# Performance work log

Hardware: AMD Instinct MI355X
Metric: run time of the kernel (lower is better)

Reference implementation:

```python
import jax, jax.numpy as jnp
import numpy as np

N = 100000      # nodes
E = 1_600_000   # edges (avg degree 16)
DIMS = [(64, 64), (64, 64), (64, 40)]  # gnn_layers [64,64,64,40]


def setup_inputs() -> dict:
    key = jax.random.key(0)
    ks = jax.random.split(key, 2 + 3 * len(DIMS))
    inp = {
        "x": jax.random.normal(ks[0], (N, DIMS[0][0]), jnp.float32),
        "edge_index": jax.random.randint(ks[1], (2, E), 0, N),
    }
    k = 2
    for i, (din, dout) in enumerate(DIMS):
        s = 1.0 / np.sqrt(din)
        inp[f"Wl{i}"] = jax.random.uniform(ks[k], (din, dout), jnp.float32, -s, s); k += 1
        inp[f"bl{i}"] = jax.random.uniform(ks[k], (dout,), jnp.float32, -s, s); k += 1
        inp[f"Wr{i}"] = jax.random.uniform(ks[k], (din, dout), jnp.float32, -s, s); k += 1
    return inp


def _sage_conv(x, src, dst, Wl, bl, Wr):
    # PyG SAGEConv (mean aggr): out = lin_l(mean_{j in N(i)} x_j) + lin_r(x_i)
    deg = jax.ops.segment_sum(jnp.ones((src.shape[0],), x.dtype), dst, num_segments=N)
    agg = jax.ops.segment_sum(x[src], dst, num_segments=N)  # [N, din] scatter-add
    agg = agg / jnp.clip(deg, 1.0)[:, None]                  # mean; isolated nodes -> 0
    return agg @ Wl + bl + x @ Wr


def reference(x, edge_index, Wl0, bl0, Wr0, Wl1, bl1, Wr1, Wl2, bl2, Wr2):
    src, dst = edge_index[0], edge_index[1]
    h = x
    params = [(Wl0, bl0, Wr0), (Wl1, bl1, Wr1), (Wl2, bl2, Wr2)]
    for i, (Wl, bl, Wr) in enumerate(params):
        h = _sage_conv(h, src, dst, Wl, bl, Wr)
        if i != len(params) - 1:
            h = jax.nn.relu(h)
            # F.dropout with training=False is identity (eval mode)
    return jax.nn.log_softmax(h, axis=1)
```

## Files before the change

### kernel.cpp

```cpp
#include <hip/hip_runtime.h>
#include <math.h>

#define ACT_RELU 0
#define ACT_LSM  1
#define BSH 8
#define MAXNB 512
#define MPAD 80

typedef __attribute__((ext_vector_type(8))) short bf16x8;
typedef __attribute__((ext_vector_type(4))) float f32x4;

__device__ __forceinline__ unsigned f2bf(float f) {
  unsigned u = __float_as_uint(f);
  u += 0x7fffu + ((u >> 16) & 1u);
  return u >> 16;
}
__device__ __forceinline__ float bflo(unsigned u) { return __uint_as_float(u << 16); }
__device__ __forceinline__ float bfhi(unsigned u) { return __uint_as_float(u & 0xffff0000u); }

__global__ void k_zero(int* __restrict__ p, int n) {
  int i = blockIdx.x * 256 + threadIdx.x;
  if (i < n) p[i] = 0;
}

__global__ void k_histB(const int* __restrict__ dst, int* __restrict__ bucket_cnt,
                        int E, int NB) {
  __shared__ int cntL[MAXNB];
  int t = threadIdx.x;
  for (int b = t; b < NB; b += 256) cntL[b] = 0;
  __syncthreads();
  int e0 = blockIdx.x * 4096;
  int e1 = min(e0 + 4096, E);
  for (int i = e0 + t; i < e1; i += 256) atomicAdd(&cntL[dst[i] >> BSH], 1);
  __syncthreads();
  for (int b = t; b < NB; b += 256)
    if (cntL[b]) atomicAdd(&bucket_cnt[b], cntL[b]);
}

__global__ void k_bscan(const int* __restrict__ bucket_cnt, int* __restrict__ bucket_base,
                        int* __restrict__ bucket_cursor, int NB) {
  __shared__ int sm[MAXNB];
  int t = threadIdx.x;
  sm[t] = (t < NB) ? bucket_cnt[t] : 0;
  __syncthreads();
  for (int off = 1; off < MAXNB; off <<= 1) {
    int x = (t >= off) ? sm[t - off] : 0;
    __syncthreads();
    sm[t] += x;
    __syncthreads();
  }
  int ex = (t == 0) ? 0 : sm[t - 1];
  if (t <= NB) bucket_base[t] = ex;
  if (t < NB) bucket_cursor[t] = ex;
}

__global__ void k_partition(const int* __restrict__ src, const int* __restrict__ dst,
                            int* __restrict__ bucket_cursor, unsigned* __restrict__ tmp,
                            int E, int NB) {
  __shared__ int cntL[MAXNB];
  __shared__ int baseL[MAXNB];
  int t = threadIdx.x;
  for (int b = t; b < NB; b += 256) cntL[b] = 0;
  __syncthreads();
  int e0 = blockIdx.x * 4096;
  int e1 = min(e0 + 4096, E);
  for (int i = e0 + t; i < e1; i += 256) atomicAdd(&cntL[dst[i] >> BSH], 1);
  __syncthreads();
  for (int b = t; b < NB; b += 256) {
    int c = cntL[b];
    baseL[b] = c ? atomicAdd(&bucket_cursor[b], c) : 0;
    cntL[b] = 0;
  }
  __syncthreads();
  for (int i = e0 + t; i < e1; i += 256) {
    int s = src[i], d = dst[i];
    int b = d >> BSH;
    int r = atomicAdd(&cntL[b], 1);
    tmp[baseL[b] + r] = ((unsigned)s << 8) | (unsigned)(d & 255);
  }
}

__global__ void __launch_bounds__(256) k_bmake(const unsigned* __restrict__ tmp,
                                               const int* __restrict__ bucket_base,
                                               int* __restrict__ row_ptr,
                                               int* __restrict__ edge_src,
                                               int N, int E, int NB) {
  __shared__ int cntL[256];
  __shared__ int scanL[256];
  int b = blockIdx.x;
  int t = threadIdx.x;
  int e0 = bucket_base[b], e1 = bucket_base[b + 1];
  cntL[t] = 0;
  __syncthreads();
  for (int i = e0 + t; i < e1; i += 256) atomicAdd(&cntL[tmp[i] & 255], 1);
  __syncthreads();
  int v = cntL[t];
  scanL[t] = v;
  __syncthreads();
  for (int off = 1; off < 256; off <<= 1) {
    int x = (t >= off) ? scanL[t - off] : 0;
    __syncthreads();
    scanL[t] += x;
    __syncthreads();
  }
  int exc = scanL[t] - v;
  int node = (b << BSH) + t;
  if (node < N) row_ptr[node] = e0 + exc;
  if (b == NB - 1 && t == 0) row_ptr[N] = E;
  __syncthreads();
  cntL[t] = e0 + exc;
  __syncthreads();
  for (int i = e0 + t; i < e1; i += 256) {
    unsigned e = tmp[i];
    int p = atomicAdd(&cntL[e & 255], 1);
    edge_src[p] = (int)(e >> 8);
  }
}

__global__ void k_hist(const int* __restrict__ dst, int* __restrict__ cnt, int E) {
  int i = blockIdx.x * blockDim.x + threadIdx.x;
  if (i < E) atomicAdd(&cnt[dst[i]], 1);
}

__global__ void k_scan_part(const int* __restrict__ cnt, int* __restrict__ bsum, int M) {
  __shared__ int sm[256];
  int t = threadIdx.x;
  int base = blockIdx.x * 2048 + t * 8;
  int s = 0;
#pragma unroll
  for (int j = 0; j < 8; ++j) { int i = base + j; if (i < M) s += cnt[i]; }
  sm[t] = s;
  __syncthreads();
  for (int off = 128; off > 0; off >>= 1) {
    if (t < off) sm[t] += sm[t + off];
    __syncthreads();
  }
  if (t == 0) bsum[blockIdx.x] = sm[0];
}

__global__ void k_scan_mid(const int* __restrict__ bsum, int* __restrict__ boff, int nb) {
  int l = threadIdx.x;
  int v = (l < nb) ? bsum[l] : 0;
  int inc = v;
  for (int off = 1; off < 64; off <<= 1) {
    int u = __shfl_up(inc, off);
    if (l >= off) inc += u;
  }
  if (l < nb) boff[l] = inc - v;
}

__global__ void k_scan_final(const int* __restrict__ cnt, const int* __restrict__ boff,
                             int* __restrict__ row_ptr, int* __restrict__ cursor, int M) {
  __shared__ int sm[256];
  int t = threadIdx.x;
  int base = blockIdx.x * 2048 + t * 8;
  int v[8];
  int s = 0;
#pragma unroll
  for (int j = 0; j < 8; ++j) { int i = base + j; v[j] = (i < M) ? cnt[i] : 0; s += v[j]; }
  sm[t] = s;
  __syncthreads();
  for (int off = 1; off < 256; off <<= 1) {
    int x = (t >= off) ? sm[t - off] : 0;
    __syncthreads();
    sm[t] += x;
    __syncthreads();
  }
  int run = boff[blockIdx.x] + sm[t] - s;
#pragma unroll
  for (int j = 0; j < 8; ++j) {
    int i = base + j;
    if (i < M) { row_ptr[i] = run; cursor[i] = run; }
    run += v[j];
  }
}

__global__ void k_fill(const int* __restrict__ src, const int* __restrict__ dst,
                       int* __restrict__ cursor, int* __restrict__ edge_src, int E) {
  int i = blockIdx.x * blockDim.x + threadIdx.x;
  if (i < E) {
    int d = dst[i];
    int p = atomicAdd(&cursor[d], 1);
    edge_src[p] = src[i];
  }
}

__global__ void __launch_bounds__(256) k_cast(const float* __restrict__ x,
                                              unsigned short* __restrict__ xb, int n) {
  int i = blockIdx.x * 256 + threadIdx.x;
  if (i * 8 < n) {
    const float4* p = (const float4*)(x + (size_t)i * 8);
    float4 a = p[0], b = p[1];
    uint4 w;
    w.x = f2bf(a.x) | (f2bf(a.y) << 16);
    w.y = f2bf(a.z) | (f2bf(a.w) << 16);
    w.z = f2bf(b.x) | (f2bf(b.y) << 16);
    w.w = f2bf(b.z) | (f2bf(b.w) << 16);
    *(uint4*)(xb + (size_t)i * 8) = w;
  }
}

__device__ __forceinline__ void prepw_one(const float* Wl, const float* Wr,
                                          unsigned short* Wb, int fi, int DOUT, int NT) {
  int k7 = fi & 7;
  int kb = (fi >> 3) & 3;
  int c16 = (fi >> 5) & 15;
  int rest = fi >> 9;
  int nt = rest % NT;
  int kb5 = rest / NT;
  int k = kb5 * 32 + kb * 8 + k7;
  int nn = nt * 16 + c16;
  float v = 0.f;
  if (nn < DOUT) v = (k < 64) ? Wl[k * DOUT + nn] : Wr[(k - 64) * DOUT + nn];
  Wb[fi] = (unsigned short)f2bf(v);
}

__global__ void k_prepw3(const float* __restrict__ Wl0, const float* __restrict__ Wr0,
                         unsigned short* __restrict__ Wb0,
                         const float* __restrict__ Wl1, const float* __restrict__ Wr1,
                         unsigned short* __restrict__ Wb1,
                         const float* __restrict__ Wl2, const float* __restrict__ Wr2,
                         unsigned short* __restrict__ Wb2) {
  int i = blockIdx.x * 256 + threadIdx.x;
  if (i < 8192) prepw_one(Wl0, Wr0, Wb0, i, 64, 4);
  else if (i < 16384) prepw_one(Wl1, Wr1, Wb1, i - 8192, 64, 4);
  else if (i < 22528) prepw_one(Wl2, Wr2, Wb2, i - 16384, 40, 3);
}

template <int DOUT, int ACT>
__global__ void __launch_bounds__(256) k_layer(const unsigned short* __restrict__ h,
                                               const int* __restrict__ row_ptr,
                                               const int* __restrict__ edge_src,
                                               const unsigned short* __restrict__ Wb,
                                               const float* __restrict__ bias,
                                               void* __restrict__ outv, int n) {
  constexpr int NT = (DOUT + 15) / 16;
  __shared__ unsigned short meanL[4][8 * MPAD];
  int t = threadIdx.x;
  int w = t >> 6, lane = t & 63;
  int r0 = (blockIdx.x * 4 + w) * 8;
  int g = lane & 7;
  int node = lane >> 3;

  {
    int i = r0 + node;
    float a[8];
#pragma unroll
    for (int c = 0; c < 8; ++c) a[c] = 0.f;
    float scale = 0.f;
    if (i < n) {
      int rp0 = row_ptr[i], rp1 = row_ptr[i + 1];
      int deg = rp1 - rp0;
      scale = (deg > 0) ? (1.0f / (float)deg) : 0.f;
      for (int base = 0; base < deg; base += 8) {
        int idx = rp0 + base + g;
        int sv = (idx < rp1) ? edge_src[idx] : 0;
        int cnt = min(8, deg - base);
        uint4 v0, v1, v2, v3, v4, v5, v6, v7;
#pragma unroll
        for (int e = 0; e < 8; ++e) {
          int s = __shfl(sv, (lane & ~7) | e);
          const uint4* p = (const uint4*)(h + (size_t)s * 64) + g;
          if (e == 0 && e < cnt) v0 = *p;
          if (e == 1 && e < cnt) v1 = *p;
          if (e == 2 && e < cnt) v2 = *p;
          if (e == 3 && e < cnt) v3 = *p;
          if (e == 4 && e < cnt) v4 = *p;
          if (e == 5 && e < cnt) v5 = *p;
          if (e == 6 && e < cnt) v6 = *p;
          if (e == 7 && e < cnt) v7 = *p;
        }
#define ACCUM(vv, ee)                                                   \
        if ((ee) < cnt) {                                               \
          a[0] += bflo(vv.x); a[1] += bfhi(vv.x);                       \
          a[2] += bflo(vv.y); a[3] += bfhi(vv.y);                       \
          a[4] += bflo(vv.z); a[5] += bfhi(vv.z);                       \
          a[6] += bflo(vv.w); a[7] += bfhi(vv.w);                       \
        }
        ACCUM(v0, 0) ACCUM(v1, 1) ACCUM(v2, 2) ACCUM(v3, 3)
        ACCUM(v4, 4) ACCUM(v5, 5) ACCUM(v6, 6) ACCUM(v7, 7)
#undef ACCUM
      }
    }
    uint4 wv;
    wv.x = f2bf(a[0] * scale) | (f2bf(a[1] * scale) << 16);
    wv.y = f2bf(a[2] * scale) | (f2bf(a[3] * scale) << 16);
    wv.z = f2bf(a[4] * scale) | (f2bf(a[5] * scale) << 16);
    wv.w = f2bf(a[6] * scale) | (f2bf(a[7] * scale) << 16);
    *(uint4*)&meanL[w][node * MPAD + g * 8] = wv;
  }
  __threadfence_block();

  int c = lane & 15;
  int c8 = c & 7;
  int kb = lane >> 4;
  bf16x8 af[4];
  af[0] = *(const bf16x8*)&meanL[w][c8 * MPAD + kb * 8];
  af[1] = *(const bf16x8*)&meanL[w][c8 * MPAD + 32 + kb * 8];
  int row = r0 + c8;
  if (row >= n) row = n - 1;
  size_t rb = (size_t)row * 64 + kb * 8;
  af[2] = *(const bf16x8*)(h + rb);
  af[3] = *(const bf16x8*)(h + rb + 32);

  f32x4 acc[NT];
#pragma unroll
  for (int nt = 0; nt < NT; ++nt) acc[nt] = (f32x4){0.f, 0.f, 0.f, 0.f};
#pragma unroll
  for (int s = 0; s < 4; ++s) {
    bf16x8 bft[NT];
#pragma unroll
    for (int nt = 0; nt < NT; ++nt)
      bft[nt] = *(const bf16x8*)&Wb[(((s * NT + nt) * 16 + c) * 4 + kb) * 8];
#pragma unroll
    for (int nt = 0; nt < NT; ++nt)
      acc[nt] = __builtin_amdgcn_mfma_f32_16x16x32_bf16(af[s], bft[nt], acc[nt], 0, 0, 0);
  }

  int rbase = r0 + kb * 4;
  bool rowv = (kb < 2);
  if (ACT == ACT_RELU) {
    unsigned short* out = (unsigned short*)outv;
#pragma unroll
    for (int nt = 0; nt < NT; ++nt) {
      float bval = bias[nt * 16 + c];
#pragma unroll
      for (int r = 0; r < 4; ++r) {
        int R = rbase + r;
        if (rowv && R < n) {
          float v = fmaxf(acc[nt][r] + bval, 0.f);
          out[(size_t)R * DOUT + nt * 16 + c] = (unsigned short)f2bf(v);
        }
      }
    }
  } else {
    float* out = (float*)outv;
    float bv[NT];
#pragma unroll
    for (int nt = 0; nt < NT; ++nt) bv[nt] = ((nt * 16 + c) < DOUT) ? bias[nt * 16 + c] : 0.f;
#pragma unroll
    for (int r = 0; r < 4; ++r) {
      int R = rbase + r;
      float v[NT];
      float m = -INFINITY;
#pragma unroll
      for (int nt = 0; nt < NT; ++nt) {
        bool valid = (nt * 16 + c) < DOUT;
        v[nt] = valid ? (acc[nt][r] + bv[nt]) : -INFINITY;
        m = fmaxf(m, v[nt]);
      }
#pragma unroll
      for (int off = 1; off < 16; off <<= 1) m = fmaxf(m, __shfl_xor(m, off));
      float es = 0.f;
#pragma unroll
      for (int nt = 0; nt < NT; ++nt)
        if ((nt * 16 + c) < DOUT) es += expf(v[nt] - m);
#pragma unroll
      for (int off = 1; off < 16; off <<= 1) es += __shfl_xor(es, off);
      float lse = logf(es);
      if (rowv && R < n) {
#pragma unroll
        for (int nt = 0; nt < NT; ++nt)
          if ((nt * 16 + c) < DOUT) out[(size_t)R * DOUT + nt * 16 + c] = v[nt] - m - lse;
      }
    }
  }
}

extern "C" void kernel_launch(void* const* d_in, const int* in_sizes, int n_in,
                              void* d_out, int out_size, void* d_ws, size_t ws_size,
                              hipStream_t stream) {
  const float* x   = (const float*)d_in[0];
  const int*   ei  = (const int*)d_in[1];
  const float* Wl0 = (const float*)d_in[2];
  const float* bl0 = (const float*)d_in[3];
  const float* Wr0 = (const float*)d_in[4];
  const float* Wl1 = (const float*)d_in[5];
  const float* bl1 = (const float*)d_in[6];
  const float* Wr1 = (const float*)d_in[7];
  const float* Wl2 = (const float*)d_in[8];
  const float* bl2 = (const float*)d_in[9];
  const float* Wr2 = (const float*)d_in[10];
  float* out = (float*)d_out;

  int N = in_sizes[0] / 64;
  int E = in_sizes[1] / 2;
  int M = N + 1;
  int NB = (N + 255) >> BSH;
  const int* src = ei;
  const int* dst = ei + E;

  char* p = (char*)d_ws;
  auto alloc = [&](size_t bytes) {
    char* r = p;
    p += (bytes + 255) & ~(size_t)255;
    return r;
  };
  int* cnt      = (int*)alloc((size_t)M * 4);
  int* row_ptr  = (int*)alloc((size_t)M * 4);
  int* cursor   = (int*)alloc((size_t)M * 4);
  int* bsum     = (int*)alloc(256 * 4);
  int* boff     = (int*)alloc(256 * 4);
  int* bk_cnt   = (int*)alloc((MAXNB + 1) * 4);
  int* bk_base  = (int*)alloc((MAXNB + 1) * 4);
  int* bk_cur   = (int*)alloc((MAXNB + 1) * 4);
  int* edge_src = (int*)alloc((size_t)E * 4);
  size_t szR1 = (size_t)E * 4 > (size_t)N * 128 ? (size_t)E * 4 : (size_t)N * 128;
  char* R1              = alloc(szR1);
  unsigned short* hbA   = (unsigned short*)alloc((size_t)N * 128);
  unsigned short* Wb0   = (unsigned short*)alloc(128 * 64 * 2);
  unsigned short* Wb1   = (unsigned short*)alloc(128 * 64 * 2);
  unsigned short* Wb2   = (unsigned short*)alloc(128 * 48 * 2);
  if ((size_t)(p - (char*)d_ws) > ws_size) return;

  bool bucketed = (NB <= MAXNB) && (N < (1 << 24));
  int eb4 = (E + 4095) / 4096;

  k_prepw3<<<(22528 + 255) / 256, 256, 0, stream>>>(Wl0, Wr0, Wb0, Wl1, Wr1, Wb1,
                                                    Wl2, Wr2, Wb2);

  if (bucketed) {
    k_zero<<<(MAXNB + 256) / 256, 256, 0, stream>>>(bk_cnt, MAXNB + 1);
    k_histB<<<eb4, 256, 0, stream>>>(dst, bk_cnt, E, NB);
    k_bscan<<<1, MAXNB, 0, stream>>>(bk_cnt, bk_base, bk_cur, NB);
    k_partition<<<eb4, 256, 0, stream>>>(src, dst, bk_cur, (unsigned*)R1, E, NB);
    k_bmake<<<NB, 256, 0, stream>>>((const unsigned*)R1, bk_base, row_ptr, edge_src, N, E, NB);
  } else {
    k_zero<<<(M + 255) / 256, 256, 0, stream>>>(cnt, M);
    k_hist<<<(E + 255) / 256, 256, 0, stream>>>(dst, cnt, E);
    int nb = (M + 2047) / 2048;
    k_scan_part<<<nb, 256, 0, stream>>>(cnt, bsum, M);
    k_scan_mid<<<1, 64, 0, stream>>>(bsum, boff, nb);
    k_scan_final<<<nb, 256, 0, stream>>>(cnt, boff, row_ptr, cursor, M);
    k_fill<<<(E + 255) / 256, 256, 0, stream>>>(src, dst, cursor, edge_src, E);
  }

  unsigned short* xb  = (unsigned short*)R1;
  unsigned short* hbB = (unsigned short*)R1;

  int cb = (N * 64 / 8 + 255) / 256;
  int gb = (N + 31) / 32;

  k_cast<<<cb, 256, 0, stream>>>(x, xb, N * 64);
  k_layer<64, ACT_RELU><<<gb, 256, 0, stream>>>(xb, row_ptr, edge_src, Wb0, bl0, hbA, N);
  k_layer<64, ACT_RELU><<<gb, 256, 0, stream>>>(hbA, row_ptr, edge_src, Wb1, bl1, hbB, N);
  k_layer<40, ACT_LSM><<<gb, 256, 0, stream>>>(hbB, row_ptr, edge_src, Wb2, bl2, out, N);
}
```

Measured before the change: 211.8 us.

## Fuse preprocessing kernels, deterministic per-block partition offsets, 16 rows per wave

The bucket-count zeroing moves into the weight-prep kernel, and the x-to-bf16 cast moves into the histogram kernel. Per-block bucket counts are now stored and prefix-scanned by a new kernel, so the partition pass no longer recounts edges or does global atomics. The temporary edge buffer gets its own allocation instead of aliasing the cast buffer, and each wave in the layer kernel now handles 16 rows, so all 16 MFMA rows are used instead of 8. The cost is an extra scan launch, more workspace for the per-block tables, and twice the gather work per wave, which may hurt latency hiding.

```diff
diff --git a/kernel.cpp b/kernel.cpp
--- a/kernel.cpp
+++ b/kernel.cpp
@@ -17,188 +17,6 @@
 }
 __device__ __forceinline__ float bflo(unsigned u) { return __uint_as_float(u << 16); }
 __device__ __forceinline__ float bfhi(unsigned u) { return __uint_as_float(u & 0xffff0000u); }
-
-__global__ void k_zero(int* __restrict__ p, int n) {
-  int i = blockIdx.x * 256 + threadIdx.x;
-  if (i < n) p[i] = 0;
-}
-
-__global__ void k_histB(const int* __restrict__ dst, int* __restrict__ bucket_cnt,
-                        int E, int NB) {
-  __shared__ int cntL[MAXNB];
-  int t = threadIdx.x;
-  for (int b = t; b < NB; b += 256) cntL[b] = 0;
-  __syncthreads();
-  int e0 = blockIdx.x * 4096;
-  int e1 = min(e0 + 4096, E);
-  for (int i = e0 + t; i < e1; i += 256) atomicAdd(&cntL[dst[i] >> BSH], 1);
-  __syncthreads();
-  for (int b = t; b < NB; b += 256)
-    if (cntL[b]) atomicAdd(&bucket_cnt[b], cntL[b]);
-}
-
-__global__ void k_bscan(const int* __restrict__ bucket_cnt, int* __restrict__ bucket_base,
-                        int* __restrict__ bucket_cursor, int NB) {
-  __shared__ int sm[MAXNB];
-  int t = threadIdx.x;
-  sm[t] = (t < NB) ? bucket_cnt[t] : 0;
-  __syncthreads();
-  for (int off = 1; off < MAXNB; off <<= 1) {
-    int x = (t >= off) ? sm[t - off] : 0;
-    __syncthreads();
-    sm[t] += x;
-    __syncthreads();
-  }
-  int ex = (t == 0) ? 0 : sm[t - 1];
-  if (t <= NB) bucket_base[t] = ex;
-  if (t < NB) bucket_cursor[t] = ex;
-}
-
-__global__ void k_partition(const int* __restrict__ src, const int* __restrict__ dst,
-                            int* __restrict__ bucket_cursor, unsigned* __restrict__ tmp,
-                            int E, int NB) {
-  __shared__ int cntL[MAXNB];
-  __shared__ int baseL[MAXNB];
-  int t = threadIdx.x;
-  for (int b = t; b < NB; b += 256) cntL[b] = 0;
-  __syncthreads();
-  int e0 = blockIdx.x * 4096;
-  int e1 = min(e0 + 4096, E);
-  for (int i = e0 + t; i < e1; i += 256) atomicAdd(&cntL[dst[i] >> BSH], 1);
-  __syncthreads();
-  for (int b = t; b < NB; b += 256) {
-    int c = cntL[b];
-    baseL[b] = c ? atomicAdd(&bucket_cursor[b], c) : 0;
-    cntL[b] = 0;
-  }
-  __syncthreads();
-  for (int i = e0 + t; i < e1; i += 256) {
-    int s = src[i], d = dst[i];
-    int b = d >> BSH;
-    int r = atomicAdd(&cntL[b], 1);
-    tmp[baseL[b] + r] = ((unsigned)s << 8) | (unsigned)(d & 255);
-  }
-}
-
-__global__ void __launch_bounds__(256) k_bmake(const unsigned* __restrict__ tmp,
-                                               const int* __restrict__ bucket_base,
-                                               int* __restrict__ row_ptr,
-                                               int* __restrict__ edge_src,
-                                               int N, int E, int NB) {
-  __shared__ int cntL[256];
-  __shared__ int scanL[256];
-  int b = blockIdx.x;
-  int t = threadIdx.x;
-  int e0 = bucket_base[b], e1 = bucket_base[b + 1];
-  cntL[t] = 0;
-  __syncthreads();
-  for (int i = e0 + t; i < e1; i += 256) atomicAdd(&cntL[tmp[i] & 255], 1);
-  __syncthreads();
-  int v = cntL[t];
-  scanL[t] = v;
-  __syncthreads();
-  for (int off = 1; off < 256; off <<= 1) {
-    int x = (t >= off) ? scanL[t - off] : 0;
-    __syncthreads();
-    scanL[t] += x;
-    __syncthreads();
-  }
-  int exc = scanL[t] - v;
-  int node = (b << BSH) + t;
-  if (node < N) row_ptr[node] = e0 + exc;
-  if (b == NB - 1 && t == 0) row_ptr[N] = E;
-  __syncthreads();
-  cntL[t] = e0 + exc;
-  __syncthreads();
-  for (int i = e0 + t; i < e1; i += 256) {
-    unsigned e = tmp[i];
-    int p = atomicAdd(&cntL[e & 255], 1);
-    edge_src[p] = (int)(e >> 8);
-  }
-}
-
-__global__ void k_hist(const int* __restrict__ dst, int* __restrict__ cnt, int E) {
-  int i = blockIdx.x * blockDim.x + threadIdx.x;
-  if (i < E) atomicAdd(&cnt[dst[i]], 1);
-}
-
-__global__ void k_scan_part(const int* __restrict__ cnt, int* __restrict__ bsum, int M) {
-  __shared__ int sm[256];
-  int t = threadIdx.x;
-  int base = blockIdx.x * 2048 + t * 8;
-  int s = 0;
-#pragma unroll
-  for (int j = 0; j < 8; ++j) { int i = base + j; if (i < M) s += cnt[i]; }
-  sm[t] = s;
-  __syncthreads();
-  for (int off = 128; off > 0; off >>= 1) {
-    if (t < off) sm[t] += sm[t + off];
-    __syncthreads();
-  }
-  if (t == 0) bsum[blockIdx.x] = sm[0];
-}
-
-__global__ void k_scan_mid(const int* __restrict__ bsum, int* __restrict__ boff, int nb) {
-  int l = threadIdx.x;
-  int v = (l < nb) ? bsum[l] : 0;
-  int inc = v;
-  for (int off = 1; off < 64; off <<= 1) {
-    int u = __shfl_up(inc, off);
-    if (l >= off) inc += u;
-  }
-  if (l < nb) boff[l] = inc - v;
-}
-
-__global__ void k_scan_final(const int* __restrict__ cnt, const int* __restrict__ boff,
-                             int* __restrict__ row_ptr, int* __restrict__ cursor, int M) {
-  __shared__ int sm[256];
-  int t = threadIdx.x;
-  int base = blockIdx.x * 2048 + t * 8;
-  int v[8];
-  int s = 0;
-#pragma unroll
-  for (int j = 0; j < 8; ++j) { int i = base + j; v[j] = (i < M) ? cnt[i] : 0; s += v[j]; }
-  sm[t] = s;
-  __syncthreads();
-  for (int off = 1; off < 256; off <<= 1) {
-    int x = (t >= off) ? sm[t - off] : 0;
-    __syncthreads();
-    sm[t] += x;
-    __syncthreads();
-  }
-  int run = boff[blockIdx.x] + sm[t] - s;
-#pragma unroll
-  for (int j = 0; j < 8; ++j) {
-    int i = base + j;
-    if (i < M) { row_ptr[i] = run; cursor[i] = run; }
-    run += v[j];
-  }
-}
-
-__global__ void k_fill(const int* __restrict__ src, const int* __restrict__ dst,
-                       int* __restrict__ cursor, int* __restrict__ edge_src, int E) {
-  int i = blockIdx.x * blockDim.x + threadIdx.x;
-  if (i < E) {
-    int d = dst[i];
-    int p = atomicAdd(&cursor[d], 1);
-    edge_src[p] = src[i];
-  }
-}
-
-__global__ void __launch_bounds__(256) k_cast(const float* __restrict__ x,
-                                              unsigned short* __restrict__ xb, int n) {
-  int i = blockIdx.x * 256 + threadIdx.x;
-  if (i * 8 < n) {
-    const float4* p = (const float4*)(x + (size_t)i * 8);
-    float4 a = p[0], b = p[1];
-    uint4 w;
-    w.x = f2bf(a.x) | (f2bf(a.y) << 16);
-    w.y = f2bf(a.z) | (f2bf(a.w) << 16);
-    w.z = f2bf(b.x) | (f2bf(b.y) << 16);
-    w.w = f2bf(b.z) | (f2bf(b.w) << 16);
-    *(uint4*)(xb + (size_t)i * 8) = w;
-  }
-}
 
 __device__ __forceinline__ void prepw_one(const float* Wl, const float* Wr,
                                           unsigned short* Wb, int fi, int DOUT, int NT) {
@@ -220,11 +38,219 @@
                          const float* __restrict__ Wl1, const float* __restrict__ Wr1,
                          unsigned short* __restrict__ Wb1,
                          const float* __restrict__ Wl2, const float* __restrict__ Wr2,
-                         unsigned short* __restrict__ Wb2) {
+                         unsigned short* __restrict__ Wb2,
+                         int* __restrict__ bk_cnt) {
   int i = blockIdx.x * 256 + threadIdx.x;
   if (i < 8192) prepw_one(Wl0, Wr0, Wb0, i, 64, 4);
   else if (i < 16384) prepw_one(Wl1, Wr1, Wb1, i - 8192, 64, 4);
   else if (i < 22528) prepw_one(Wl2, Wr2, Wb2, i - 16384, 40, 3);
+  if (i <= MAXNB) bk_cnt[i] = 0;
+}
+
+__global__ void __launch_bounds__(256) k_histB(const int* __restrict__ dst,
+                                               const float* __restrict__ x,
+                                               unsigned short* __restrict__ xb,
+                                               int* __restrict__ bucket_cnt,
+                                               int* __restrict__ bk_blk,
+                                               int E, int NB, int NBLK, int nx8) {
+  __shared__ int cntL[MAXNB];
+  int t = threadIdx.x;
+  for (int i = blockIdx.x * 256 + t; i < nx8; i += gridDim.x * 256) {
+    const float4* p = (const float4*)(x + (size_t)i * 8);
+    float4 a = p[0], b = p[1];
+    uint4 w;
+    w.x = f2bf(a.x) | (f2bf(a.y) << 16);
+    w.y = f2bf(a.z) | (f2bf(a.w) << 16);
+    w.z = f2bf(b.x) | (f2bf(b.y) << 16);
+    w.w = f2bf(b.z) | (f2bf(b.w) << 16);
+    *(uint4*)(xb + (size_t)i * 8) = w;
+  }
+  for (int b = t; b < NB; b += 256) cntL[b] = 0;
+  __syncthreads();
+  int e0 = blockIdx.x * 4096;
+  int e1 = min(e0 + 4096, E);
+  for (int i = e0 + t; i < e1; i += 256) atomicAdd(&cntL[dst[i] >> BSH], 1);
+  __syncthreads();
+  for (int b = t; b < NB; b += 256) {
+    int c = cntL[b];
+    bk_blk[b * NBLK + blockIdx.x] = c;
+    if (c) atomicAdd(&bucket_cnt[b], c);
+  }
+}
+
+__global__ void k_bscan(const int* __restrict__ bucket_cnt, int* __restrict__ bucket_base,
+                        int NB) {
+  __shared__ int sm[MAXNB];
+  int t = threadIdx.x;
+  sm[t] = (t < NB) ? bucket_cnt[t] : 0;
+  __syncthreads();
+  for (int off = 1; off < MAXNB; off <<= 1) {
+    int x = (t >= off) ? sm[t - off] : 0;
+    __syncthreads();
+    sm[t] += x;
+    __syncthreads();
+  }
+  int ex = (t == 0) ? 0 : sm[t - 1];
+  if (t <= NB) bucket_base[t] = ex;
+}
+
+__global__ void k_bscan2(const int* __restrict__ bk_blk, const int* __restrict__ bucket_base,
+                         int* __restrict__ base_blk, int NBLK) {
+  __shared__ int sm[512];
+  int b = blockIdx.x;
+  int t = threadIdx.x;
+  int v = (t < NBLK) ? bk_blk[b * NBLK + t] : 0;
+  sm[t] = v;
+  __syncthreads();
+  for (int off = 1; off < 512; off <<= 1) {
+    int x = (t >= off) ? sm[t - off] : 0;
+    __syncthreads();
+    sm[t] += x;
+    __syncthreads();
+  }
+  if (t < NBLK) base_blk[b * NBLK + t] = bucket_base[b] + sm[t] - v;
+}
+
+__global__ void k_partition(const int* __restrict__ src, const int* __restrict__ dst,
+                            const int* __restrict__ base_blk, unsigned* __restrict__ tmp,
+                            int E, int NB, int NBLK) {
+  __shared__ int curL[MAXNB];
+  int t = threadIdx.x;
+  for (int b = t; b < NB; b += 256) curL[b] = base_blk[b * NBLK + blockIdx.x];
+  __syncthreads();
+  int e0 = blockIdx.x * 4096;
+  int e1 = min(e0 + 4096, E);
+  for (int i = e0 + t; i < e1; i += 256) {
+    int s = src[i], d = dst[i];
+    int b = d >> BSH;
+    int r = atomicAdd(&curL[b], 1);
+    tmp[r] = ((unsigned)s << 8) | (unsigned)(d & 255);
+  }
+}
+
+__global__ void __launch_bounds__(256) k_bmake(const unsigned* __restrict__ tmp,
+                                               const int* __restrict__ bucket_base,
+                                               int* __restrict__ row_ptr,
+                                               int* __restrict__ edge_src,
+                                               int N, int E, int NB) {
+  __shared__ int cntL[256];
+  __shared__ int scanL[256];
+  int b = blockIdx.x;
+  int t = threadIdx.x;
+  int e0 = bucket_base[b], e1 = bucket_base[b + 1];
+  cntL[t] = 0;
+  __syncthreads();
+  for (int i = e0 + t; i < e1; i += 256) atomicAdd(&cntL[tmp[i] & 255], 1);
+  __syncthreads();
+  int v = cntL[t];
+  scanL[t] = v;
+  __syncthreads();
+  for (int off = 1; off < 256; off <<= 1) {
+    int x = (t >= off) ? scanL[t - off] : 0;
+    __syncthreads();
+    scanL[t] += x;
+    __syncthreads();
+  }
+  int exc = scanL[t] - v;
+  int node = (b << BSH) + t;
+  if (node < N) row_ptr[node] = e0 + exc;
+  if (b == NB - 1 && t == 0) row_ptr[N] = E;
+  __syncthreads();
+  cntL[t] = e0 + exc;
+  __syncthreads();
+  for (int i = e0 + t; i < e1; i += 256) {
+    unsigned e = tmp[i];
+    int p = atomicAdd(&cntL[e & 255], 1);
+    edge_src[p] = (int)(e >> 8);
+  }
+}
+
+__global__ void k_zero(int* __restrict__ p, int n) {
+  int i = blockIdx.x * 256 + threadIdx.x;
+  if (i < n) p[i] = 0;
+}
+
+__global__ void k_hist(const int* __restrict__ dst, int* __restrict__ cnt, int E) {
+  int i = blockIdx.x * blockDim.x + threadIdx.x;
+  if (i < E) atomicAdd(&cnt[dst[i]], 1);
+}
+
+__global__ void k_scan_part(const int* __restrict__ cnt, int* __restrict__ bsum, int M) {
+  __shared__ int sm[256];
+  int t = threadIdx.x;
+  int base = blockIdx.x * 2048 + t * 8;
+  int s = 0;
+#pragma unroll
+  for (int j = 0; j < 8; ++j) { int i = base + j; if (i < M) s += cnt[i]; }
+  sm[t] = s;
+  __syncthreads();
+  for (int off = 128; off > 0; off >>= 1) {
+    if (t < off) sm[t] += sm[t + off];
+    __syncthreads();
+  }
+  if (t == 0) bsum[blockIdx.x] = sm[0];
+}
+
+__global__ void k_scan_mid(const int* __restrict__ bsum, int* __restrict__ boff, int nb) {
+  int l = threadIdx.x;
+  int v = (l < nb) ? bsum[l] : 0;
+  int inc = v;
+  for (int off = 1; off < 64; off <<= 1) {
+    int u = __shfl_up(inc, off);
+    if (l >= off) inc += u;
+  }
+  if (l < nb) boff[l] = inc - v;
+}
+
+__global__ void k_scan_final(const int* __restrict__ cnt, const int* __restrict__ boff,
+                             int* __restrict__ row_ptr, int* __restrict__ cursor, int M) {
+  __shared__ int sm[256];
+  int t = threadIdx.x;
+  int base = blockIdx.x * 2048 + t * 8;
+  int v[8];
+  int s = 0;
+#pragma unroll
+  for (int j = 0; j < 8; ++j) { int i = base + j; v[j] = (i < M) ? cnt[i] : 0; s += v[j]; }
+  sm[t] = s;
+  __syncthreads();
+  for (int off = 1; off < 256; off <<= 1) {
+    int x = (t >= off) ? sm[t - off] : 0;
+    __syncthreads();
+    sm[t] += x;
+    __syncthreads();
+  }
+  int run = boff[blockIdx.x] + sm[t] - s;
+#pragma unroll
+  for (int j = 0; j < 8; ++j) {
+    int i = base + j;
+    if (i < M) { row_ptr[i] = run; cursor[i] = run; }
+    run += v[j];
+  }
+}
+
+__global__ void k_fill(const int* __restrict__ src, const int* __restrict__ dst,
+                       int* __restrict__ cursor, int* __restrict__ edge_src, int E) {
+  int i = blockIdx.x * blockDim.x + threadIdx.x;
+  if (i < E) {
+    int d = dst[i];
+    int p = atomicAdd(&cursor[d], 1);
+    edge_src[p] = src[i];
+  }
+}
+
+__global__ void __launch_bounds__(256) k_cast(const float* __restrict__ x,
+                                              unsigned short* __restrict__ xb, int n) {
+  int i = blockIdx.x * 256 + threadIdx.x;
+  if (i * 8 < n) {
+    const float4* p = (const float4*)(x + (size_t)i * 8);
+    float4 a = p[0], b = p[1];
+    uint4 w;
+    w.x = f2bf(a.x) | (f2bf(a.y) << 16);
+    w.y = f2bf(a.z) | (f2bf(a.w) << 16);
+    w.z = f2bf(b.x) | (f2bf(b.y) << 16);
+    w.w = f2bf(b.z) | (f2bf(b.w) << 16);
+    *(uint4*)(xb + (size_t)i * 8) = w;
+  }
 }
 
 template <int DOUT, int ACT>
@@ -235,14 +261,14 @@
                                                const float* __restrict__ bias,
                                                void* __restrict__ outv, int n) {
   constexpr int NT = (DOUT + 15) / 16;
-  __shared__ unsigned short meanL[4][8 * MPAD];
+  __shared__ unsigned short meanL[4][16 * MPAD];
   int t = threadIdx.x;
   int w = t >> 6, lane = t & 63;
-  int r0 = (blockIdx.x * 4 + w) * 8;
+  int r0 = (blockIdx.x * 4 + w) * 16;
   int g = lane & 7;
-  int node = lane >> 3;
-
-  {
+
+  for (int half = 0; half < 2; ++half) {
+    int node = half * 8 + (lane >> 3);
     int i = r0 + node;
     float a[8];
 #pragma unroll
@@ -292,12 +318,11 @@
   __threadfence_block();
 
   int c = lane & 15;
-  int c8 = c & 7;
   int kb = lane >> 4;
   bf16x8 af[4];
-  af[0] = *(const bf16x8*)&meanL[w][c8 * MPAD + kb * 8];
-  af[1] = *(const bf16x8*)&meanL[w][c8 * MPAD + 32 + kb * 8];
-  int row = r0 + c8;
+  af[0] = *(const bf16x8*)&meanL[w][c * MPAD + kb * 8];
+  af[1] = *(const bf16x8*)&meanL[w][c * MPAD + 32 + kb * 8];
+  int row = r0 + c;
   if (row >= n) row = n - 1;
   size_t rb = (size_t)row * 64 + kb * 8;
   af[2] = *(const bf16x8*)(h + rb);
@@ -318,7 +343,6 @@
   }
 
   int rbase = r0 + kb * 4;
-  bool rowv = (kb < 2);
   if (ACT == ACT_RELU) {
     unsigned short* out = (unsigned short*)outv;
 #pragma unroll
@@ -327,7 +351,7 @@
 #pragma unroll
       for (int r = 0; r < 4; ++r) {
         int R = rbase + r;
-        if (rowv && R < n) {
+        if (R < n) {
           float v = fmaxf(acc[nt][r] + bval, 0.f);
           out[(size_t)R * DOUT + nt * 16 + c] = (unsigned short)f2bf(v);
         }
@@ -358,7 +382,7 @@
 #pragma unroll
       for (int off = 1; off < 16; off <<= 1) es += __shfl_xor(es, off);
       float lse = logf(es);
-      if (rowv && R < n) {
+      if (R < n) {
 #pragma unroll
         for (int nt = 0; nt < NT; ++nt)
           if ((nt * 16 + c) < DOUT) out[(size_t)R * DOUT + nt * 16 + c] = v[nt] - m - lse;
@@ -387,6 +411,7 @@
   int E = in_sizes[1] / 2;
   int M = N + 1;
   int NB = (N + 255) >> BSH;
+  int NBLK = (E + 4095) / 4096;
   const int* src = ei;
   const int* dst = ei + E;
 
@@ -403,28 +428,31 @@
   int* boff     = (int*)alloc(256 * 4);
   int* bk_cnt   = (int*)alloc((MAXNB + 1) * 4);
   int* bk_base  = (int*)alloc((MAXNB + 1) * 4);
-  int* bk_cur   = (int*)alloc((MAXNB + 1) * 4);
   int* edge_src = (int*)alloc((size_t)E * 4);
-  size_t szR1 = (size_t)E * 4 > (size_t)N * 128 ? (size_t)E * 4 : (size_t)N * 128;
-  char* R1              = alloc(szR1);
-  unsigned short* hbA   = (unsigned short*)alloc((size_t)N * 128);
-  unsigned short* Wb0   = (unsigned short*)alloc(128 * 64 * 2);
-  unsigned short* Wb1   = (unsigned short*)alloc(128 * 64 * 2);
-  unsigned short* Wb2   = (unsigned short*)alloc(128 * 48 * 2);
+  unsigned* tmp = (unsigned*)alloc((size_t)E * 4);
+  int* bk_blk   = (int*)alloc((size_t)MAXNB * (size_t)NBLK * 4);
+  int* base_blk = (int*)alloc((size_t)MAXNB * (size_t)NBLK * 4);
+  unsigned short* R1  = (unsigned short*)alloc((size_t)N * 128);
+  unsigned short* hbA = (unsigned short*)alloc((size_t)N * 128);
+  unsigned short* Wb0 = (unsigned short*)alloc(128 * 64 * 2);
+  unsigned short* Wb1 = (unsigned short*)alloc(128 * 64 * 2);
+  unsigned short* Wb2 = (unsigned short*)alloc(128 * 48 * 2);
   if ((size_t)(p - (char*)d_ws) > ws_size) return;
 
-  bool bucketed = (NB <= MAXNB) && (N < (1 << 24));
-  int eb4 = (E + 4095) / 4096;
+  bool bucketed = (NB <= MAXNB) && (N < (1 << 24)) && (NBLK <= 512);
+
+  unsigned short* xb  = R1;
+  unsigned short* hbB = R1;
 
   k_prepw3<<<(22528 + 255) / 256, 256, 0, stream>>>(Wl0, Wr0, Wb0, Wl1, Wr1, Wb1,
-                                                    Wl2, Wr2, Wb2);
+                                                    Wl2, Wr2, Wb2, bk_cnt);
 
   if (bucketed) {
-    k_zero<<<(MAXNB + 256) / 256, 256, 0, stream>>>(bk_cnt, MAXNB + 1);
-    k_histB<<<eb4, 256, 0, stream>>>(dst, bk_cnt, E, NB);
-    k_bscan<<<1, MAXNB, 0, stream>>>(bk_cnt, bk_base, bk_cur, NB);
-    k_partition<<<eb4, 256, 0, stream>>>(src, dst, bk_cur, (unsigned*)R1, E, NB);
-    k_bmake<<<NB, 256, 0, stream>>>((const unsigned*)R1, bk_base, row_ptr, edge_src, N, E, NB);
+    k_histB<<<NBLK, 256, 0, stream>>>(dst, x, xb, bk_cnt, bk_blk, E, NB, NBLK, N * 8);
+    k_bscan<<<1, MAXNB, 0, stream>>>(bk_cnt, bk_base, NB);
+    k_bscan2<<<NB, 512, 0, stream>>>(bk_blk, bk_base, base_blk, NBLK);
+    k_partition<<<NBLK, 256, 0, stream>>>(src, dst, base_blk, tmp, E, NB, NBLK);
+    k_bmake<<<NB, 256, 0, stream>>>(tmp, bk_base, row_ptr, edge_src, N, E, NB);
   } else {
     k_zero<<<(M + 255) / 256, 256, 0, stream>>>(cnt, M);
     k_hist<<<(E + 255) / 256, 256, 0, stream>>>(dst, cnt, E);
@@ -433,15 +461,10 @@
     k_scan_mid<<<1, 64, 0, stream>>>(bsum, boff, nb);
     k_scan_final<<<nb, 256, 0, stream>>>(cnt, boff, row_ptr, cursor, M);
     k_fill<<<(E + 255) / 256, 256, 0, stream>>>(src, dst, cursor, edge_src, E);
-  }
-
-  unsigned short* xb  = (unsigned short*)R1;
-  unsigned short* hbB = (unsigned short*)R1;
-
-  int cb = (N * 64 / 8 + 255) / 256;
-  int gb = (N + 31) / 32;
-
-  k_cast<<<cb, 256, 0, stream>>>(x, xb, N * 64);
+    k_cast<<<(N * 8 + 255) / 256, 256, 0, stream>>>(x, xb, N * 64);
+  }
+
+  int gb = (N + 63) / 64;
   k_layer<64, ACT_RELU><<<gb, 256, 0, stream>>>(xb, row_ptr, edge_src, Wb0, bl0, hbA, N);
   k_layer<64, ACT_RELU><<<gb, 256, 0, stream>>>(hbA, row_ptr, edge_src, Wb1, bl1, hbB, N);
   k_layer<40, ACT_LSM><<<gb, 256, 0, stream>>>(hbB, row_ptr, edge_src, Wb2, bl2, out, N);
```

New measurement: 184.3 us (median of 2 runs). 1.15x faster.
